# Kernel optimization log

Hardware: AMD Instinct MI355X
Metric: run time of the kernel (lower is better)

## Reference

```python
import jax, jax.numpy as jnp
import numpy as np
import math

N = 50000
E = 1600000
A = 100          # num_atoms
H = 64           # hidden_dim / node_dim
L = 5            # num_layers
NB = 8           # num_basis
LMAX = 2
CUTOFF = 5.0


def setup_inputs() -> dict:
    key = jax.random.key(0)
    ks = jax.random.split(key, 32)
    s = 0.05
    inp = {
        'atomic_numbers': jax.random.randint(ks[0], (N,), 0, A),
        'pos': jax.random.normal(ks[1], (N, 3), jnp.float32) * 2.0,
        'edge_index': jax.random.randint(ks[2], (2, E), 0, N),
        # GaussianBasis widths
        'widths': jnp.ones((NB,), jnp.float32) * 0.5,
        # node embedding
        'embed': jax.random.normal(ks[3], (A, H), jnp.float32),
        # per-layer params, stacked on leading layer dim
        'rad_w1': jax.random.normal(ks[4], (L, NB, H), jnp.float32) * s,
        'rad_b1': jnp.zeros((L, H), jnp.float32),
        'rad_w2': jax.random.normal(ks[5], (L, H, H * (LMAX + 1)), jnp.float32) * s,
        'rad_b2': jnp.zeros((L, H * (LMAX + 1)), jnp.float32),
        'self_w': jax.random.normal(ks[6], (L, H, H), jnp.float32) * s,
        'self_b': jnp.zeros((L, H), jnp.float32),
        'proj_w': jax.random.normal(ks[7], (L, 2 * H, H), jnp.float32) * s,
        'proj_b': jnp.zeros((L, H), jnp.float32),
        'mlp_w1': jax.random.normal(ks[8], (L, H, 2 * H), jnp.float32) * s,
        'mlp_b1': jnp.zeros((L, 2 * H), jnp.float32),
        'mlp_w2': jax.random.normal(ks[9], (L, 2 * H, H), jnp.float32) * s,
        'mlp_b2': jnp.zeros((L, H), jnp.float32),
        'ln_g': jnp.ones((L, H), jnp.float32),
        'ln_b': jnp.zeros((L, H), jnp.float32),
        # readout MLP
        'ro_w1': jax.random.normal(ks[10], (H, H), jnp.float32) * s,
        'ro_b1': jnp.zeros((H,), jnp.float32),
        'ro_w2': jax.random.normal(ks[11], (H, H // 2), jnp.float32) * s,
        'ro_b2': jnp.zeros((H // 2,), jnp.float32),
        'ro_w3': jax.random.normal(ks[12], (H // 2, 1), jnp.float32) * s,
        'ro_b3': jnp.zeros((1,), jnp.float32),
        # per-species reference energies
        'atomic_e': jax.random.normal(ks[13], (A, 1), jnp.float32) * s,
    }
    return inp


def _layer_norm(x, g, b, eps=1e-5):
    mu = jnp.mean(x, axis=-1, keepdims=True)
    var = jnp.var(x, axis=-1, keepdims=True)
    return (x - mu) * jax.lax.rsqrt(var + eps) * g + b


def _spherical_harmonics(edge_vec):
    # real SH up to lmax=2, [E, 9] (computed for fidelity; unused by conv math)
    r = jnp.clip(jnp.linalg.norm(edge_vec, axis=-1), 1e-8, None)
    x, y, z = edge_vec[:, 0] / r, edge_vec[:, 1] / r, edge_vec[:, 2] / r
    x2, y2, z2 = x * x, y * y, z * z
    return jnp.stack([
        jnp.full_like(x, 0.28209479177387814),
        -0.4886025119029199 * y, 0.4886025119029199 * z, -0.4886025119029199 * x,
        1.0925484305920792 * x * y, -1.0925484305920792 * y * z,
        0.94617469575756 * z2 - 0.31539156525252 * (x2 + y2),
        -1.0925484305920792 * x * z, 0.5462742152960396 * (x2 - y2),
    ], axis=-1)


def _forward(atomic_numbers, pos, edge_index, widths, embed,
             rad_w1, rad_b1, rad_w2, rad_b2, self_w, self_b, proj_w, proj_b,
             mlp_w1, mlp_b1, mlp_w2, mlp_b2, ln_g, ln_b,
             ro_w1, ro_b1, ro_w2, ro_b2, ro_w3, ro_b3, atomic_e):
    n = pos.shape[0]
    row, col = edge_index[0], edge_index[1]
    edge_vec = pos[col] - pos[row]                          # [E,3]
    edge_len = jnp.linalg.norm(edge_vec, axis=-1, keepdims=True)  # [E,1]

    # GaussianBasis
    xr = edge_len / CUTOFF
    cut = 0.5 * (jnp.cos(xr * math.pi) + 1.0)
    cut = cut * (edge_len < CUTOFF).astype(jnp.float32)     # [E,1]
    centers = jnp.linspace(0.0, CUTOFF, NB)
    diff = edge_len - centers                               # [E,NB]
    edge_rbf = jnp.exp(-0.5 * (diff / jnp.clip(widths, 0.1, None)) ** 2) * cut

    edge_sh = _spherical_harmonics(edge_vec)  # computed but unused, as in source

    feats = embed[atomic_numbers]                           # [N,H]
    for i in range(L):
        # radial net -> per-edge weights [E, H*(lmax+1)]
        w = jax.nn.silu(edge_rbf @ rad_w1[i] + rad_b1[i]) @ rad_w2[i] + rad_b2[i]
        # messages: node_j[:,:,None] * w.view(E,H,lmax+1) summed over last dim
        # == node_j * w.reshape(E,H,lmax+1).sum(-1)
        wsum = w.reshape(-1, H, LMAX + 1).sum(axis=-1)      # [E,H]
        messages = feats[col] * wsum                        # gather + multiply
        agg = jax.ops.segment_sum(messages, row, num_segments=n)  # scatter-add
        self_out = feats @ self_w[i] + self_b[i]
        conv_out = jnp.concatenate([self_out, agg], axis=-1) @ proj_w[i] + proj_b[i]
        upd = jax.nn.silu(conv_out @ mlp_w1[i] + mlp_b1[i]) @ mlp_w2[i] + mlp_b2[i]
        feats = _layer_norm(feats + upd, ln_g[i], ln_b[i])

    h = jax.nn.silu(feats @ ro_w1 + ro_b1)
    h = jax.nn.silu(h @ ro_w2 + ro_b2)
    atomic_energies = h @ ro_w3 + ro_b3                     # [N,1]
    atomic_energies = atomic_energies + atomic_e[atomic_numbers]
    return atomic_energies.sum()                            # batch=None path


def reference(atomic_numbers, pos, edge_index, widths, embed,
              rad_w1, rad_b1, rad_w2, rad_b2, self_w, self_b, proj_w, proj_b,
              mlp_w1, mlp_b1, mlp_w2, mlp_b2, ln_g, ln_b,
              ro_w1, ro_b1, ro_w2, ro_b2, ro_w3, ro_b3, atomic_e):
    return _forward(atomic_numbers, pos, edge_index, widths, embed,
                    rad_w1, rad_b1, rad_w2, rad_b2, self_w, self_b, proj_w, proj_b,
                    mlp_w1, mlp_b1, mlp_w2, mlp_b2, ln_g, ln_b,
                    ro_w1, ro_b1, ro_w2, ro_b2, ro_w3, ro_b3, atomic_e)
```

## Files before the change

kernel.cpp:

```cpp
#include <hip/hip_runtime.h>
#include <hip/hip_fp16.h>
#include <math.h>

constexpr int N_NODES = 50000;
constexpr int N_EDGES = 1600000;
constexpr int HDIM    = 64;
constexpr int NLAYER  = 5;
constexpr int NBASIS  = 8;
constexpr int TLUT    = 256;
constexpr float CUT_R = 5.0f;
constexpr float PI_F  = 3.14159265358979f;

constexpr int NBKT = 196;
constexpr int BCAP = 9216;
constexpr int TILE = 2048;

typedef __attribute__((ext_vector_type(8))) short short8;
typedef __attribute__((ext_vector_type(4))) float f32x4;
#define MFMA16 __builtin_amdgcn_mfma_f32_16x16x32_bf16

__device__ __forceinline__ float siluf(float x) { return x / (1.0f + __expf(-x)); }

__device__ __forceinline__ unsigned int f2bf(float x) {
    unsigned int b = __float_as_uint(x);
    return (b + 0x7fffu + ((b >> 16) & 1u)) >> 16;
}
__device__ __forceinline__ float bf_lo(unsigned int u) { return __uint_as_float(u << 16); }
__device__ __forceinline__ float bf_hi(unsigned int u) { return __uint_as_float(u & 0xffff0000u); }

__device__ __forceinline__ unsigned int f2e5(float x) {
    unsigned short b = __half_as_ushort(__float2half(x));
    return ((unsigned int)b + 0x7Fu + ((b >> 8) & 1u)) >> 8;
}
__device__ __forceinline__ float e5f(unsigned int u8) {
    return __half2float(__ushort_as_half((unsigned short)(u8 << 8)));
}

__device__ __forceinline__ int blockScan256Excl(int cv, int tid, int* wtot) {
    int v = cv;
    int lane = tid & 63;
    #pragma unroll
    for (int off = 1; off < 64; off <<= 1) {
        int t = __shfl_up(v, off, 64);
        if (lane >= off) v += t;
    }
    if (lane == 63) wtot[tid >> 6] = v;
    __syncthreads();
    int pre = 0;
    #pragma unroll
    for (int w = 0; w < 4; ++w)
        if (w < (tid >> 6)) pre += wtot[w];
    __syncthreads();
    return v + pre - cv;
}


__global__ void k_embed(const int* __restrict__ an, const float* __restrict__ embed,
                        float* __restrict__ feats, unsigned short* __restrict__ featsbf,
                        unsigned char* __restrict__ featsf8) {
    int i = blockIdx.x * blockDim.x + threadIdx.x;
    if (i >= N_NODES * HDIM) return;
    int node = i >> 6, h = i & 63;
    float v = embed[an[node] * HDIM + h];
    feats[i] = v;
    featsbf[i] = (unsigned short)f2bf(v);
    featsf8[i] = (unsigned char)f2e5(v);
}

__global__ __launch_bounds__(256) void k_binA(const int* __restrict__ row,
                                              const int* __restrict__ col,
                                              const float* __restrict__ pos,
                                              int* __restrict__ btail,
                                              unsigned int* __restrict__ binned) {
    __shared__ unsigned int ent[TILE];
    __shared__ short bb[TILE];
    __shared__ unsigned int sorted[TILE];
    __shared__ short sortedB[TILE];
    __shared__ int cnt[256], cnt2[256], base[256], gbase[256];
    __shared__ int wtot[4];
    const int tid = threadIdx.x;
    const int t0  = blockIdx.x * TILE;
    const int nv  = min(TILE, N_EDGES - t0);

    cnt[tid] = 0;
    __syncthreads();

    #pragma unroll
    for (int i = 0; i < TILE / 256; ++i) {
        int idx = i * 256 + tid;
        if (idx < nv) {
            int e = t0 + idx;
            int r = row[e], c = col[e];
            float dx = pos[c * 3 + 0] - pos[r * 3 + 0];
            float dy = pos[c * 3 + 1] - pos[r * 3 + 1];
            float dz = pos[c * 3 + 2] - pos[r * 3 + 2];
            float len = sqrtf(dx * dx + dy * dy + dz * dz);
            float t = len * ((float)(TLUT - 1) / CUT_R);
            t = fminf(t, (float)(TLUT - 1));
            unsigned int nn = (unsigned int)(t + 0.5f);
            if (nn > TLUT - 1) nn = TLUT - 1;
            ent[idx] = ((unsigned int)c << 16) | (nn << 8) | ((unsigned int)r & 255u);
            int b = r >> 8;
            bb[idx] = (short)b;
            atomicAdd(&cnt[b], 1);
        }
    }
    __syncthreads();
    int cv = cnt[tid];
    int excl = blockScan256Excl(cv, tid, wtot);
    base[tid] = excl;
    if (tid < NBKT && cv > 0) gbase[tid] = atomicAdd(&btail[tid], cv);
    cnt2[tid] = excl;
    __syncthreads();
    #pragma unroll
    for (int i = 0; i < TILE / 256; ++i) {
        int idx = i * 256 + tid;
        if (idx < nv) {
            int b = bb[idx];
            int p = atomicAdd(&cnt2[b], 1);
            sorted[p]  = ent[idx];
            sortedB[p] = (short)b;
        }
    }
    __syncthreads();
    for (int s = tid; s < nv; s += 256) {
        int b = sortedB[s];
        binned[(size_t)b * BCAP + gbase[b] + (s - base[b])] = sorted[s];
    }
}

__global__ void k_scanB(const int* __restrict__ btail, int* __restrict__ bbase) {
    __shared__ int wtot[4];
    int t = threadIdx.x;
    int v = (t < NBKT) ? btail[t] : 0;
    int excl = blockScan256Excl(v, t, wtot);
    if (t < NBKT) bbase[t] = excl;
}

__global__ __launch_bounds__(256) void k_binB(const unsigned int* __restrict__ binned,
                                              const int* __restrict__ btail,
                                              const int* __restrict__ bbase,
                                              int* __restrict__ starts,
                                              unsigned int* __restrict__ erec) {
    __shared__ int hist[256];
    __shared__ int cur[256];
    __shared__ int wtot[4];
    const int b = blockIdx.x;
    const int node0 = b << 8;
    const int t = threadIdx.x;
    hist[t] = 0;
    __syncthreads();
    const int cnt = btail[b];
    const unsigned int* src = binned + (size_t)b * BCAP;
    for (int s = t; s < cnt; s += 256)
        atomicAdd(&hist[src[s] & 255u], 1);
    __syncthreads();
    int h = hist[t];
    int excl = bbase[b] + blockScan256Excl(h, t, wtot);
    int n = node0 + t;
    if (n < N_NODES) starts[n] = excl;
    if (b == 0 && t == 0) starts[N_NODES] = N_EDGES;
    cur[t] = excl;
    __syncthreads();
    for (int s = t; s < cnt; s += 256) {
        unsigned int p = src[s];
        int pp = atomicAdd(&cur[p & 255u], 1);
        erec[pp] = p;
    }
}

__global__ void k_prep(const float* __restrict__ rad_w2, const float* __restrict__ self_w,
                       const float* __restrict__ proj_w,
                       const float* __restrict__ rad_b2, const float* __restrict__ self_b,
                       const float* __restrict__ proj_b,
                       float* __restrict__ W2s, float* __restrict__ Wsp,
                       float* __restrict__ b2s, float* __restrict__ bsp) {
    int i = blockIdx.x * blockDim.x + threadIdx.x;
    if (i < NLAYER * HDIM * HDIM) {
        int l = i / (HDIM * HDIM); int rem = i % (HDIM * HDIM);
        int k = rem / HDIM; int h = rem % HDIM;
        const float* w = rad_w2 + ((size_t)l * HDIM + k) * (HDIM * 3) + h * 3;
        W2s[i] = w[0] + w[1] + w[2];
        const float* sw = self_w + ((size_t)l * HDIM + k) * HDIM;
        const float* pw = proj_w + (size_t)l * 2 * HDIM * HDIM;
        float acc = 0.f;
        for (int m = 0; m < HDIM; ++m) acc += sw[m] * pw[m * HDIM + h];
        Wsp[i] = acc;
    } else {
        int i2 = i - NLAYER * HDIM * HDIM;
        if (i2 >= NLAYER * HDIM) return;
        int l = i2 / HDIM, h = i2 % HDIM;
        const float* rb2 = rad_b2 + l * HDIM * 3 + h * 3;
        b2s[i2] = rb2[0] + rb2[1] + rb2[2];
        float acc = proj_b[l * HDIM + h];
        const float* pw = proj_w + (size_t)l * 2 * HDIM * HDIM;
        const float* sb = self_b + l * HDIM;
        for (int m = 0; m < HDIM; ++m) acc += sb[m] * pw[m * HDIM + h];
        bsp[i2] = acc;
    }
}

__global__ void k_wtr(const float* __restrict__ Wsp, const float* __restrict__ proj_w,
                      const float* __restrict__ mlp_w1, const float* __restrict__ mlp_w2,
                      const float* __restrict__ ro_w1, const float* __restrict__ ro_w2,
                      unsigned short* __restrict__ WspT, unsigned short* __restrict__ PbT,
                      unsigned short* __restrict__ W1T, unsigned short* __restrict__ W2T,
                      unsigned short* __restrict__ Ro1T, unsigned short* __restrict__ Ro2T) {
    int i = blockIdx.x * blockDim.x + threadIdx.x;
    if (i < NLAYER * 24576) {
        int l = i / 24576, off = i % 24576;
        if (off < 4096) {
            int n = off >> 6, k = off & 63;
            WspT[(size_t)l * 4096 + off] = (unsigned short)f2bf(Wsp[(size_t)l * 4096 + k * 64 + n]);
        } else if (off < 8192) {
            int o = off - 4096; int n = o >> 6, k = o & 63;
            PbT[(size_t)l * 4096 + o] =
                (unsigned short)f2bf(proj_w[(size_t)l * 8192 + (64 + k) * 64 + n]);
        } else if (off < 16384) {
            int o = off - 8192; int n = o >> 6, k = o & 63;
            W1T[(size_t)l * 8192 + o] = (unsigned short)f2bf(mlp_w1[(size_t)l * 8192 + k * 128 + n]);
        } else {
            int o = off - 16384; int n = o >> 7, k = o & 127;
            W2T[(size_t)l * 8192 + o] = (unsigned short)f2bf(mlp_w2[(size_t)l * 8192 + k * 64 + n]);
        }
    } else {
        int i2 = i - NLAYER * 24576;
        if (i2 >= 6144) return;
        if (i2 < 4096) {
            int n = i2 >> 6, k = i2 & 63;
            Ro1T[i2] = (unsigned short)f2bf(ro_w1[k * 64 + n]);
        } else {
            int o = i2 - 4096; int n = o >> 6, k = o & 63;
            Ro2T[o] = (unsigned short)f2bf(ro_w2[k * 32 + n]);
        }
    }
}

__global__ void k_lut(const float* __restrict__ widths, const float* __restrict__ rad_w1,
                      const float* __restrict__ rad_b1, const float* __restrict__ W2s,
                      const float* __restrict__ b2s, unsigned short* __restrict__ lutB) {
    int bid = blockIdx.x;
    int l = bid / TLUT, t = bid % TLUT;
    int h = threadIdx.x;
    __shared__ float h1s[HDIM];
    float len = (float)t * (CUT_R / (float)(TLUT - 1));
    float cut = 0.0f;
    if (len < CUT_R) cut = 0.5f * (cosf(len * (PI_F / CUT_R)) + 1.0f);
    float acc = rad_b1[l * HDIM + h];
    for (int b = 0; b < NBASIS; ++b) {
        float wb = fmaxf(widths[b], 0.1f);
        float center = (float)b * (CUT_R / (float)(NBASIS - 1));
        float d = (len - center) / wb;
        float rbf = __expf(-0.5f * d * d) * cut;
        acc += rbf * rad_w1[(l * NBASIS + b) * HDIM + h];
    }
    h1s[h] = siluf(acc);
    __syncthreads();
    float o = b2s[l * HDIM + h];
    const float* w2 = W2s + (size_t)l * HDIM * HDIM;
    for (int k = 0; k < HDIM; ++k) o += h1s[k] * w2[k * HDIM + h];
    lutB[(size_t)bid * HDIM + h] = (unsigned short)f2bf(o);
}


__global__ __launch_bounds__(256) void k_agg(const uint2* __restrict__ featsf8_2,
                                             const uint4* __restrict__ lutB4_l,
                                             const int* __restrict__ starts,
                                             const unsigned int* __restrict__ erec,
                                             uint4* __restrict__ aggbf4) {
    int wid  = (blockIdx.x * blockDim.x + threadIdx.x) >> 6;
    int lane = threadIdx.x & 63;
    int slot = lane >> 3;
    int j    = lane & 7;
    if (wid >= N_NODES) return;
    int e0 = starts[wid], e1 = starts[wid + 1];
    float a0 = 0, a1 = 0, a2 = 0, a3 = 0, a4 = 0, a5 = 0, a6 = 0, a7 = 0;
    #pragma unroll 2
    for (int e = e0 + slot; e < e1; e += 8) {
        unsigned int rec = erec[e];
        int c  = rec >> 16;
        int i0 = (rec >> 8) & 255;
        uint4 qw = lutB4_l[i0 * 8 + j];
        uint2 fb = featsf8_2[(size_t)c * 8 + j];
        a0 += e5f(fb.x & 255u)         * bf_lo(qw.x);
        a1 += e5f((fb.x >> 8) & 255u)  * bf_hi(qw.x);
        a2 += e5f((fb.x >> 16) & 255u) * bf_lo(qw.y);
        a3 += e5f(fb.x >> 24)          * bf_hi(qw.y);
        a4 += e5f(fb.y & 255u)         * bf_lo(qw.z);
        a5 += e5f((fb.y >> 8) & 255u)  * bf_hi(qw.z);
        a6 += e5f((fb.y >> 16) & 255u) * bf_lo(qw.w);
        a7 += e5f(fb.y >> 24)          * bf_hi(qw.w);
    }
    #pragma unroll
    for (int off = 8; off < 64; off <<= 1) {
        a0 += __shfl_xor(a0, off, 64);  a1 += __shfl_xor(a1, off, 64);
        a2 += __shfl_xor(a2, off, 64);  a3 += __shfl_xor(a3, off, 64);
        a4 += __shfl_xor(a4, off, 64);  a5 += __shfl_xor(a5, off, 64);
        a6 += __shfl_xor(a6, off, 64);  a7 += __shfl_xor(a7, off, 64);
    }
    if (slot == 0) {
        uint4 o;
        o.x = f2bf(a0) | (f2bf(a1) << 16);
        o.y = f2bf(a2) | (f2bf(a3) << 16);
        o.z = f2bf(a4) | (f2bf(a5) << 16);
        o.w = f2bf(a6) | (f2bf(a7) << 16);
        aggbf4[(size_t)wid * 8 + j] = o;
    }
}

constexpr int BP = 72;
__global__ __launch_bounds__(256) void k_node(float* __restrict__ feats,
        unsigned short* __restrict__ featsbf,
        unsigned char* __restrict__ featsf8,
        const unsigned short* __restrict__ aggbf,
        const unsigned short* __restrict__ WspT_l, const unsigned short* __restrict__ PbT_l,
        const unsigned short* __restrict__ W1T_l, const unsigned short* __restrict__ W2T_l,
        const float* __restrict__ bsp_l,
        const float* __restrict__ mlp_b1_l, const float* __restrict__ mlp_b2_l,
        const float* __restrict__ ln_g_l, const float* __restrict__ ln_b_l) {
    __shared__ unsigned short P[64 * BP];
    __shared__ unsigned short Q[64 * BP];
    __shared__ unsigned short S[64 * BP];
    const int tid  = threadIdx.x;
    const int lane = tid & 63;
    const int wib  = tid >> 6;
    const int mt   = __builtin_amdgcn_readfirstlane(wib);
    const int nb0  = blockIdx.x * 64;
    const int colL = lane & 15;
    const int kgrp = lane >> 4;

    #pragma unroll 4
    for (int i = 0; i < 16; ++i) {
        int r  = wib + i * 4;
        int nd = nb0 + r; nd = (nd < N_NODES) ? nd : (N_NODES - 1);
        P[r * BP + lane] = featsbf[(size_t)nd * 64 + lane];
        Q[r * BP + lane] = aggbf[(size_t)nd * 64 + lane];
    }
    __syncthreads();

    f32x4 acc[4];
    #pragma unroll
    for (int nt = 0; nt < 4; ++nt) {
        float b = bsp_l[nt * 16 + colL];
        acc[nt][0] = b; acc[nt][1] = b; acc[nt][2] = b; acc[nt][3] = b;
    }
    #pragma unroll
    for (int kb = 0; kb < 2; ++kb) {
        short8 ax = *(const short8*)&P[(mt * 16 + colL) * BP + kb * 32 + kgrp * 8];
        short8 aa = *(const short8*)&Q[(mt * 16 + colL) * BP + kb * 32 + kgrp * 8];
        #pragma unroll
        for (int nt = 0; nt < 4; ++nt) {
            short8 bw = *(const short8*)&WspT_l[(nt * 16 + colL) * 64 + kb * 32 + kgrp * 8];
            acc[nt] = MFMA16(ax, bw, acc[nt], 0, 0, 0);
            short8 bp = *(const short8*)&PbT_l[(nt * 16 + colL) * 64 + kb * 32 + kgrp * 8];
            acc[nt] = MFMA16(aa, bp, acc[nt], 0, 0, 0);
        }
    }
    __syncthreads();
    #pragma unroll
    for (int nt = 0; nt < 4; ++nt)
        #pragma unroll
        for (int j = 0; j < 4; ++j)
            P[(mt * 16 + kgrp * 4 + j) * BP + nt * 16 + colL] = (unsigned short)f2bf(acc[nt][j]);
    __syncthreads();

    {
        f32x4 m[8];
        #pragma unroll
        for (int nt = 0; nt < 8; ++nt) {
            float b = mlp_b1_l[nt * 16 + colL];
            m[nt][0] = b; m[nt][1] = b; m[nt][2] = b; m[nt][3] = b;
        }
        #pragma unroll
        for (int kb = 0; kb < 2; ++kb) {
            short8 ac = *(const short8*)&P[(mt * 16 + colL) * BP + kb * 32 + kgrp * 8];
            #pragma unroll
            for (int nt = 0; nt < 8; ++nt) {
                short8 bw = *(const short8*)&W1T_l[(nt * 16 + colL) * 64 + kb * 32 + kgrp * 8];
                m[nt] = MFMA16(ac, bw, m[nt], 0, 0, 0);
            }
        }
        __syncthreads();
        #pragma unroll
        for (int nt = 0; nt < 4; ++nt)
            #pragma unroll
            for (int j = 0; j < 4; ++j)
                Q[(mt * 16 + kgrp * 4 + j) * BP + nt * 16 + colL] =
                    (unsigned short)f2bf(siluf(m[nt][j]));
        #pragma unroll
        for (int nt = 4; nt < 8; ++nt)
            #pragma unroll
            for (int j = 0; j < 4; ++j)
                S[(mt * 16 + kgrp * 4 + j) * BP + (nt - 4) * 16 + colL] =
                    (unsigned short)f2bf(siluf(m[nt][j]));
    }
    __syncthreads();

    f32x4 u[4];
    #pragma unroll
    for (int nt = 0; nt < 4; ++nt) {
        float b = mlp_b2_l[nt * 16 + colL];
        u[nt][0] = b; u[nt][1] = b; u[nt][2] = b; u[nt][3] = b;
    }
    #pragma unroll
    for (int kb = 0; kb < 4; ++kb) {
        short8 am = (kb < 2)
            ? *(const short8*)&Q[(mt * 16 + colL) * BP + kb * 32 + kgrp * 8]
            : *(const short8*)&S[(mt * 16 + colL) * BP + (kb - 2) * 32 + kgrp * 8];
        #pragma unroll
        for (int nt = 0; nt < 4; ++nt) {
            short8 bw = *(const short8*)&W2T_l[(nt * 16 + colL) * 128 + kb * 32 + kgrp * 8];
            u[nt] = MFMA16(am, bw, u[nt], 0, 0, 0);
        }
    }

    float y[4][4];
    float s1[4] = {0, 0, 0, 0}, s2[4] = {0, 0, 0, 0};
    #pragma unroll
    for (int j = 0; j < 4; ++j) {
        int node = nb0 + mt * 16 + kgrp * 4 + j;
        int nds  = (node < N_NODES) ? node : (N_NODES - 1);
        #pragma unroll
        for (int nt = 0; nt < 4; ++nt) {
            float v = feats[(size_t)nds * 64 + nt * 16 + colL] + u[nt][j];
            y[nt][j] = v;
            s1[j] += v; s2[j] += v * v;
        }
    }
    #pragma unroll
    for (int off = 1; off < 16; off <<= 1) {
        #pragma unroll
        for (int j = 0; j < 4; ++j) {
            s1[j] += __shfl_xor(s1[j], off, 64);
            s2[j] += __shfl_xor(s2[j], off, 64);
        }
    }
    float gv[4], bv[4];
    #pragma unroll
    for (int nt = 0; nt < 4; ++nt) {
        gv[nt] = ln_g_l[nt * 16 + colL];
        bv[nt] = ln_b_l[nt * 16 + colL];
    }
    #pragma unroll
    for (int j = 0; j < 4; ++j) {
        int node = nb0 + mt * 16 + kgrp * 4 + j;
        if (node >= N_NODES) continue;
        float mu  = s1[j] * (1.0f / 64.0f);
        float var = s2[j] * (1.0f / 64.0f) - mu * mu;
        float rr  = rsqrtf(var + 1e-5f);
        #pragma unroll
        for (int nt = 0; nt < 4; ++nt) {
            float o = (y[nt][j] - mu) * rr * gv[nt] + bv[nt];
            size_t idx = (size_t)node * 64 + nt * 16 + colL;
            feats[idx]   = o;
            featsbf[idx] = (unsigned short)f2bf(o);
            featsf8[idx] = (unsigned char)f2e5(o);
        }
    }
}


__global__ __launch_bounds__(256) void k_readout(const unsigned short* __restrict__ featsbf,
        const int* __restrict__ an,
        const unsigned short* __restrict__ Ro1T, const unsigned short* __restrict__ Ro2T,
        const float* __restrict__ ro_b1, const float* __restrict__ ro_b2,
        const float* __restrict__ ro_w3, const float* __restrict__ ro_b3,
        const float* __restrict__ atomic_e, float* __restrict__ blockpart) {
    __shared__ unsigned short P[64 * BP];
    __shared__ unsigned short Q[64 * BP];
    __shared__ float sred[256];
    const int tid  = threadIdx.x;
    const int lane = tid & 63;
    const int wib  = tid >> 6;
    const int mt   = __builtin_amdgcn_readfirstlane(wib);
    const int nb0  = blockIdx.x * 64;
    const int colL = lane & 15;
    const int kgrp = lane >> 4;

    #pragma unroll 4
    for (int i = 0; i < 16; ++i) {
        int r  = wib + i * 4;
        int nd = nb0 + r; nd = (nd < N_NODES) ? nd : (N_NODES - 1);
        P[r * BP + lane] = featsbf[(size_t)nd * 64 + lane];
    }
    __syncthreads();

    {
        f32x4 m[4];
        #pragma unroll
        for (int nt = 0; nt < 4; ++nt) {
            float b = ro_b1[nt * 16 + colL];
            m[nt][0] = b; m[nt][1] = b; m[nt][2] = b; m[nt][3] = b;
        }
        #pragma unroll
        for (int kb = 0; kb < 2; ++kb) {
            short8 ax = *(const short8*)&P[(mt * 16 + colL) * BP + kb * 32 + kgrp * 8];
            #pragma unroll
            for (int nt = 0; nt < 4; ++nt) {
                short8 bw = *(const short8*)&Ro1T[(nt * 16 + colL) * 64 + kb * 32 + kgrp * 8];
                m[nt] = MFMA16(ax, bw, m[nt], 0, 0, 0);
            }
        }
        __syncthreads();
        #pragma unroll
        for (int nt = 0; nt < 4; ++nt)
            #pragma unroll
            for (int j = 0; j < 4; ++j)
                Q[(mt * 16 + kgrp * 4 + j) * BP + nt * 16 + colL] =
                    (unsigned short)f2bf(siluf(m[nt][j]));
    }
    __syncthreads();

    f32x4 u[2];
    #pragma unroll
    for (int nt = 0; nt < 2; ++nt) {
        float b = ro_b2[nt * 16 + colL];
        u[nt][0] = b; u[nt][1] = b; u[nt][2] = b; u[nt][3] = b;
    }
    #pragma unroll
    for (int kb = 0; kb < 2; ++kb) {
        short8 am = *(const short8*)&Q[(mt * 16 + colL) * BP + kb * 32 + kgrp * 8];
        #pragma unroll
        for (int nt = 0; nt < 2; ++nt) {
            short8 bw = *(const short8*)&Ro2T[(nt * 16 + colL) * 64 + kb * 32 + kgrp * 8];
            u[nt] = MFMA16(am, bw, u[nt], 0, 0, 0);
        }
    }
    float w3[2];
    #pragma unroll
    for (int nt = 0; nt < 2; ++nt) w3[nt] = ro_w3[nt * 16 + colL];
    float part = 0.0f;
    #pragma unroll
    for (int j = 0; j < 4; ++j) {
        float c = siluf(u[0][j]) * w3[0] + siluf(u[1][j]) * w3[1];
        #pragma unroll
        for (int off = 1; off < 16; off <<= 1) c += __shfl_xor(c, off, 64);
        int node = nb0 + mt * 16 + kgrp * 4 + j;
        if (colL == 0 && node < N_NODES)
            part += c + ro_b3[0] + atomic_e[an[node]];
    }
    sred[tid] = part;
    __syncthreads();
    for (int off = 128; off > 0; off >>= 1) {
        if (tid < off) sred[tid] += sred[tid + off];
        __syncthreads();
    }
    if (tid == 0) blockpart[blockIdx.x] = sred[0];
}

__global__ void k_final(const float* __restrict__ blockpart, int nb, float* __restrict__ out) {
    __shared__ float s[256];
    float acc = 0.f;
    for (int i = threadIdx.x; i < nb; i += 256) acc += blockpart[i];
    s[threadIdx.x] = acc; __syncthreads();
    for (int off = 128; off > 0; off >>= 1) {
        if (threadIdx.x < off) s[threadIdx.x] += s[threadIdx.x + off];
        __syncthreads();
    }
    if (threadIdx.x == 0) out[0] = s[0];
}


extern "C" void kernel_launch(void* const* d_in, const int* in_sizes, int n_in,
                              void* d_out, int out_size, void* d_ws, size_t ws_size,
                              hipStream_t stream) {
    const int*   an       = (const int*)  d_in[0];
    const float* pos      = (const float*)d_in[1];
    const int*   edge     = (const int*)  d_in[2];
    const float* widths   = (const float*)d_in[3];
    const float* embed    = (const float*)d_in[4];
    const float* rad_w1   = (const float*)d_in[5];
    const float* rad_b1   = (const float*)d_in[6];
    const float* rad_w2   = (const float*)d_in[7];
    const float* rad_b2   = (const float*)d_in[8];
    const float* self_w   = (const float*)d_in[9];
    const float* self_b   = (const float*)d_in[10];
    const float* proj_w   = (const float*)d_in[11];
    const float* proj_b   = (const float*)d_in[12];
    const float* mlp_w1   = (const float*)d_in[13];
    const float* mlp_b1   = (const float*)d_in[14];
    const float* mlp_w2   = (const float*)d_in[15];
    const float* mlp_b2   = (const float*)d_in[16];
    const float* ln_g     = (const float*)d_in[17];
    const float* ln_b     = (const float*)d_in[18];
    const float* ro_w1    = (const float*)d_in[19];
    const float* ro_b1    = (const float*)d_in[20];
    const float* ro_w2    = (const float*)d_in[21];
    const float* ro_b2    = (const float*)d_in[22];
    const float* ro_w3    = (const float*)d_in[23];
    const float* ro_b3    = (const float*)d_in[24];
    const float* atomic_e = (const float*)d_in[25];

    char* w = (char*)d_ws;
    auto alloc = [&](size_t bytes) { char* p = w; w += (bytes + 255) & ~(size_t)255; return p; };
    float* feats     = (float*)alloc(sizeof(float) * N_NODES * HDIM);
    unsigned short* featsbf = (unsigned short*)alloc(sizeof(unsigned short) * N_NODES * HDIM);
    unsigned char* featsf8  = (unsigned char*)alloc(sizeof(unsigned char) * N_NODES * HDIM);
    unsigned short* aggbf   = (unsigned short*)alloc(sizeof(unsigned short) * N_NODES * HDIM);
    unsigned short* lutB = (unsigned short*)alloc(sizeof(unsigned short) * NLAYER * TLUT * HDIM);
    float* W2s       = (float*)alloc(sizeof(float) * NLAYER * HDIM * HDIM);
    float* b2s       = (float*)alloc(sizeof(float) * NLAYER * HDIM);
    float* Wsp       = (float*)alloc(sizeof(float) * NLAYER * HDIM * HDIM);
    float* bsp       = (float*)alloc(sizeof(float) * NLAYER * HDIM);
    unsigned short* WspT = (unsigned short*)alloc(sizeof(unsigned short) * NLAYER * 4096);
    unsigned short* PbT  = (unsigned short*)alloc(sizeof(unsigned short) * NLAYER * 4096);
    unsigned short* W1T  = (unsigned short*)alloc(sizeof(unsigned short) * NLAYER * 8192);
    unsigned short* W2T  = (unsigned short*)alloc(sizeof(unsigned short) * NLAYER * 8192);
    unsigned short* Ro1T = (unsigned short*)alloc(sizeof(unsigned short) * 4096);
    unsigned short* Ro2T = (unsigned short*)alloc(sizeof(unsigned short) * 2048);
    unsigned int* erec = (unsigned int*)alloc(sizeof(unsigned int) * N_EDGES);
    unsigned int* binned = (unsigned int*)alloc(sizeof(unsigned int) * (size_t)NBKT * BCAP);
    int*   btail     = (int*)  alloc(sizeof(int) * 256);
    int*   bbase     = (int*)  alloc(sizeof(int) * 256);
    int*   starts    = (int*)  alloc(sizeof(int) * (N_NODES + 1));
    float* blockpart = (float*)alloc(sizeof(float) * 1024);
    (void)ws_size; (void)in_sizes; (void)n_in; (void)out_size;

    const int* erow = edge;
    const int* ecol = edge + N_EDGES;

    hipMemsetAsync(btail, 0, sizeof(int) * 256, stream);
    k_embed<<<12500, 256, 0, stream>>>(an, embed, feats, featsbf, featsf8);
    k_binA<<<(N_EDGES + TILE - 1) / TILE, 256, 0, stream>>>(erow, ecol, pos, btail, binned);
    k_scanB<<<1, 256, 0, stream>>>(btail, bbase);
    k_binB<<<NBKT, 256, 0, stream>>>(binned, btail, bbase, starts, erec);
    k_prep<<<(NLAYER * HDIM * HDIM + NLAYER * HDIM + 255) / 256, 256, 0, stream>>>(
        rad_w2, self_w, proj_w, rad_b2, self_b, proj_b, W2s, Wsp, b2s, bsp);
    k_wtr<<<(NLAYER * 24576 + 6144 + 255) / 256, 256, 0, stream>>>(
        Wsp, proj_w, mlp_w1, mlp_w2, ro_w1, ro_w2, WspT, PbT, W1T, W2T, Ro1T, Ro2T);
    k_lut<<<NLAYER * TLUT, 64, 0, stream>>>(widths, rad_w1, rad_b1, W2s, b2s, lutB);

    for (int l = 0; l < NLAYER; ++l) {
        k_agg<<<12500, 256, 0, stream>>>((const uint2*)featsf8,
                                         (const uint4*)(lutB + (size_t)l * TLUT * HDIM),
                                         starts, erec, (uint4*)aggbf);
        k_node<<<782, 256, 0, stream>>>(feats, featsbf, featsf8, aggbf,
            WspT + (size_t)l * 4096, PbT + (size_t)l * 4096,
            W1T + (size_t)l * 8192, W2T + (size_t)l * 8192,
            bsp + l * HDIM, mlp_b1 + l * 2 * HDIM, mlp_b2 + l * HDIM,
            ln_g + l * HDIM, ln_b + l * HDIM);
    }

    k_readout<<<782, 256, 0, stream>>>(featsbf, an, Ro1T, Ro2T, ro_b1, ro_b2,
                                       ro_w3, ro_b3, atomic_e, blockpart);
    k_final<<<1, 256, 0, stream>>>(blockpart, 782, (float*)d_out);
}
```

Before: 401.8 us.

## Drop fp32 feature buffer and split edge geometry into separate kernel

Removes the fp32 feats array. The layer-norm residual is now read from the bf16 copy already staged in shared memory, which saves a 12.8MB read and a 12.8MB write per layer. Edge length and LUT-index computation moves out of k_binA into a separate fully parallel k_edge kernel, which writes packed records and bucket bytes for binA to read. The residual path loses precision because it now uses bf16, and the extra edge kernel adds an intermediate global round trip.

Result: no change. 395.9 us (-1.5%).

```diff
diff --git a/kernel.cpp b/kernel.cpp
--- a/kernel.cpp
+++ b/kernel.cpp
@@ -56,20 +56,36 @@
 
 
 __global__ void k_embed(const int* __restrict__ an, const float* __restrict__ embed,
-                        float* __restrict__ feats, unsigned short* __restrict__ featsbf,
+                        unsigned short* __restrict__ featsbf,
                         unsigned char* __restrict__ featsf8) {
     int i = blockIdx.x * blockDim.x + threadIdx.x;
     if (i >= N_NODES * HDIM) return;
     int node = i >> 6, h = i & 63;
     float v = embed[an[node] * HDIM + h];
-    feats[i] = v;
     featsbf[i] = (unsigned short)f2bf(v);
     featsf8[i] = (unsigned char)f2e5(v);
 }
 
-__global__ __launch_bounds__(256) void k_binA(const int* __restrict__ row,
-                                              const int* __restrict__ col,
-                                              const float* __restrict__ pos,
+__global__ void k_edge(const int* __restrict__ row, const int* __restrict__ col,
+                       const float* __restrict__ pos,
+                       unsigned int* __restrict__ rec4, unsigned char* __restrict__ bkt) {
+    int e = blockIdx.x * blockDim.x + threadIdx.x;
+    if (e >= N_EDGES) return;
+    int r = row[e], c = col[e];
+    float dx = pos[c * 3 + 0] - pos[r * 3 + 0];
+    float dy = pos[c * 3 + 1] - pos[r * 3 + 1];
+    float dz = pos[c * 3 + 2] - pos[r * 3 + 2];
+    float len = sqrtf(dx * dx + dy * dy + dz * dz);
+    float t = len * ((float)(TLUT - 1) / CUT_R);
+    t = fminf(t, (float)(TLUT - 1));
+    unsigned int nn = (unsigned int)(t + 0.5f);
+    if (nn > TLUT - 1) nn = TLUT - 1;
+    rec4[e] = ((unsigned int)c << 16) | (nn << 8) | ((unsigned int)r & 255u);
+    bkt[e]  = (unsigned char)(r >> 8);
+}
+
+__global__ __launch_bounds__(256) void k_binA(const unsigned int* __restrict__ rec4,
+                                              const unsigned char* __restrict__ bkt,
                                               int* __restrict__ btail,
                                               unsigned int* __restrict__ binned) {
     __shared__ unsigned int ent[TILE];
@@ -89,18 +105,8 @@
     for (int i = 0; i < TILE / 256; ++i) {
         int idx = i * 256 + tid;
         if (idx < nv) {
-            int e = t0 + idx;
-            int r = row[e], c = col[e];
-            float dx = pos[c * 3 + 0] - pos[r * 3 + 0];
-            float dy = pos[c * 3 + 1] - pos[r * 3 + 1];
-            float dz = pos[c * 3 + 2] - pos[r * 3 + 2];
-            float len = sqrtf(dx * dx + dy * dy + dz * dz);
-            float t = len * ((float)(TLUT - 1) / CUT_R);
-            t = fminf(t, (float)(TLUT - 1));
-            unsigned int nn = (unsigned int)(t + 0.5f);
-            if (nn > TLUT - 1) nn = TLUT - 1;
-            ent[idx] = ((unsigned int)c << 16) | (nn << 8) | ((unsigned int)r & 255u);
-            int b = r >> 8;
+            ent[idx] = rec4[t0 + idx];
+            int b = bkt[t0 + idx];
             bb[idx] = (short)b;
             atomicAdd(&cnt[b], 1);
         }
@@ -309,7 +315,7 @@
 }
 
 constexpr int BP = 72;
-__global__ __launch_bounds__(256) void k_node(float* __restrict__ feats,
+__global__ __launch_bounds__(256) void k_node(
         unsigned short* __restrict__ featsbf,
         unsigned char* __restrict__ featsf8,
         const unsigned short* __restrict__ aggbf,
@@ -338,6 +344,13 @@
     }
     __syncthreads();
 
+    float xres[4][4];
+    #pragma unroll
+    for (int j = 0; j < 4; ++j)
+        #pragma unroll
+        for (int nt = 0; nt < 4; ++nt)
+            xres[nt][j] = bf_lo(P[(mt * 16 + kgrp * 4 + j) * BP + nt * 16 + colL]);
+
     f32x4 acc[4];
     #pragma unroll
     for (int nt = 0; nt < 4; ++nt) {
@@ -418,11 +431,9 @@
     float s1[4] = {0, 0, 0, 0}, s2[4] = {0, 0, 0, 0};
     #pragma unroll
     for (int j = 0; j < 4; ++j) {
-        int node = nb0 + mt * 16 + kgrp * 4 + j;
-        int nds  = (node < N_NODES) ? node : (N_NODES - 1);
         #pragma unroll
         for (int nt = 0; nt < 4; ++nt) {
-            float v = feats[(size_t)nds * 64 + nt * 16 + colL] + u[nt][j];
+            float v = xres[nt][j] + u[nt][j];
             y[nt][j] = v;
             s1[j] += v; s2[j] += v * v;
         }
@@ -452,7 +463,6 @@
         for (int nt = 0; nt < 4; ++nt) {
             float o = (y[nt][j] - mu) * rr * gv[nt] + bv[nt];
             size_t idx = (size_t)node * 64 + nt * 16 + colL;
-            feats[idx]   = o;
             featsbf[idx] = (unsigned short)f2bf(o);
             featsf8[idx] = (unsigned char)f2e5(o);
         }
@@ -593,7 +603,6 @@
 
     char* w = (char*)d_ws;
     auto alloc = [&](size_t bytes) { char* p = w; w += (bytes + 255) & ~(size_t)255; return p; };
-    float* feats     = (float*)alloc(sizeof(float) * N_NODES * HDIM);
     unsigned short* featsbf = (unsigned short*)alloc(sizeof(unsigned short) * N_NODES * HDIM);
     unsigned char* featsf8  = (unsigned char*)alloc(sizeof(unsigned char) * N_NODES * HDIM);
     unsigned short* aggbf   = (unsigned short*)alloc(sizeof(unsigned short) * N_NODES * HDIM);
@@ -609,6 +618,8 @@
     unsigned short* Ro1T = (unsigned short*)alloc(sizeof(unsigned short) * 4096);
     unsigned short* Ro2T = (unsigned short*)alloc(sizeof(unsigned short) * 2048);
     unsigned int* erec = (unsigned int*)alloc(sizeof(unsigned int) * N_EDGES);
+    unsigned int* rec4 = (unsigned int*)alloc(sizeof(unsigned int) * N_EDGES);
+    unsigned char* bkt = (unsigned char*)alloc(sizeof(unsigned char) * N_EDGES);
     unsigned int* binned = (unsigned int*)alloc(sizeof(unsigned int) * (size_t)NBKT * BCAP);
     int*   btail     = (int*)  alloc(sizeof(int) * 256);
     int*   bbase     = (int*)  alloc(sizeof(int) * 256);
@@ -620,8 +631,9 @@
     const int* ecol = edge + N_EDGES;
 
     hipMemsetAsync(btail, 0, sizeof(int) * 256, stream);
-    k_embed<<<12500, 256, 0, stream>>>(an, embed, feats, featsbf, featsf8);
-    k_binA<<<(N_EDGES + TILE - 1) / TILE, 256, 0, stream>>>(erow, ecol, pos, btail, binned);
+    k_embed<<<12500, 256, 0, stream>>>(an, embed, featsbf, featsf8);
+    k_edge<<<(N_EDGES + 255) / 256, 256, 0, stream>>>(erow, ecol, pos, rec4, bkt);
+    k_binA<<<(N_EDGES + TILE - 1) / TILE, 256, 0, stream>>>(rec4, bkt, btail, binned);
     k_scanB<<<1, 256, 0, stream>>>(btail, bbase);
     k_binB<<<NBKT, 256, 0, stream>>>(binned, btail, bbase, starts, erec);
     k_prep<<<(NLAYER * HDIM * HDIM + NLAYER * HDIM + 255) / 256, 256, 0, stream>>>(
@@ -634,7 +646,7 @@
         k_agg<<<12500, 256, 0, stream>>>((const uint2*)featsf8,
                                          (const uint4*)(lutB + (size_t)l * TLUT * HDIM),
                                          starts, erec, (uint4*)aggbf);
-        k_node<<<782, 256, 0, stream>>>(feats, featsbf, featsf8, aggbf,
+        k_node<<<782, 256, 0, stream>>>(featsbf, featsf8, aggbf,
             WspT + (size_t)l * 4096, PbT + (size_t)l * 4096,
             W1T + (size_t)l * 8192, W2T + (size_t)l * 8192,
             bsp + l * HDIM, mlp_b1 + l * 2 * HDIM, mlp_b2 + l * HDIM,
```
